# Optimization experiments

Hardware: AMD Instinct MI355X
Metric: run time of the kernel (lower is better)

Reference implementation:

```python
import jax, jax.numpy as jnp
import numpy as np

B, S, D = 32, 512, 768
EPS = 1e-8  # torch CosineSimilarity eps

def setup_inputs() -> dict:
    key = jax.random.key(0)
    k1, k2, k3, k4 = jax.random.split(key, 4)
    emb1 = jax.random.normal(k1, (B, S, D), jnp.float32)
    emb2 = jax.random.normal(k2, (B, S, D), jnp.float32)
    mask1 = jax.random.randint(k3, (B, S), 0, 2).astype(jnp.int32)
    mask2 = jax.random.randint(k4, (B, S), 0, 2).astype(jnp.int32)
    return {"emb1": emb1, "emb2": emb2, "mask1": mask1, "mask2": mask2}

def reference(emb1, emb2, mask1, mask2):
    # normalize token embeddings (cosine sim = dot of unit vectors)
    n1 = emb1 / jnp.maximum(jnp.linalg.norm(emb1, axis=-1, keepdims=True), EPS)
    n2 = emb2 / jnp.maximum(jnp.linalg.norm(emb2, axis=-1, keepdims=True), EPS)
    # full pairwise cosine similarity: [B, S1, S2]
    sim = jnp.einsum('bid,bjd->bij', n1, n2)
    m1 = mask1.astype(sim.dtype)
    m2 = mask2.astype(sim.dtype)
    valid = m1[:, :, None] * m2[:, None, :]
    neg_inf = jnp.asarray(-jnp.inf, sim.dtype)
    masked = jnp.where(valid > 0, sim, neg_inf)
    # row max over valid cols; rows with no valid token contribute 0
    row_max = jnp.where(m1 > 0, jnp.max(masked, axis=2), 0.0)  # [B, S1]
    col_max = jnp.where(m2 > 0, jnp.max(masked, axis=1), 0.0)  # [B, S2]
    denom = jnp.sum(m1, axis=1) + jnp.sum(m2, axis=1)          # n1 + n2
    score = (jnp.sum(row_max, axis=1) + jnp.sum(col_max, axis=1)) / jnp.maximum(denom, 1.0)
    return score  # [B]
```

## Files before the change

kernel.cpp:

```cpp
#include <hip/hip_runtime.h>

#define BB 32
#define SS 512
#define DD 768
#define NROW (BB * SS)

typedef float f32x4 __attribute__((ext_vector_type(4)));
typedef short bf16x8 __attribute__((ext_vector_type(8)));

__device__ __forceinline__ unsigned fkey(float f) {
  unsigned u = __float_as_uint(f);
  return (u & 0x80000000u) ? ~u : (u | 0x80000000u);
}
__device__ __forceinline__ float fdecode(unsigned k) {
  return __uint_as_float((k & 0x80000000u) ? (k & 0x7fffffffu) : ~k);
}
__device__ __forceinline__ unsigned short cvt_bf16(float f) {
  unsigned u = __float_as_uint(f);
  u += 0x7fffu + ((u >> 16) & 1u);
  return (unsigned short)(u >> 16);
}

__global__ __launch_bounds__(256) void norm_cvt_kernel(
    const float* __restrict__ emb1, const float* __restrict__ emb2,
    unsigned short* __restrict__ wsA, unsigned short* __restrict__ wsB,
    unsigned* __restrict__ rowkey, unsigned* __restrict__ colkey) {
  int wave = blockIdx.x * 4 + (threadIdx.x >> 6);
  int lane = threadIdx.x & 63;
  int half = wave >> 14;
  int r = wave & (NROW - 1);
  const float* src = (half ? emb2 : emb1) + (size_t)r * DD;
  float4 v[3];
  float s = 0.f;
#pragma unroll
  for (int q = 0; q < 3; ++q) {
    v[q] = ((const float4*)src)[q * 64 + lane];
    s += v[q].x * v[q].x + v[q].y * v[q].y + v[q].z * v[q].z + v[q].w * v[q].w;
  }
#pragma unroll
  for (int m = 1; m < 64; m <<= 1) s += __shfl_xor(s, m);
  float inv = 1.0f / fmaxf(sqrtf(s), 1e-8f);
  unsigned short* dst = (half ? wsB : wsA) + (size_t)r * DD;
  int base = ((lane >> 4) << 6) + (((((lane >> 1) & 7) ^ (r & 7))) << 3) + ((lane & 1) << 2);
#pragma unroll
  for (int q = 0; q < 3; ++q) {
    ushort4 u;
    u.x = cvt_bf16(v[q].x * inv); u.y = cvt_bf16(v[q].y * inv);
    u.z = cvt_bf16(v[q].z * inv); u.w = cvt_bf16(v[q].w * inv);
    *(ushort4*)(dst + q * 256 + base) = u;
  }
  if (lane == 0) {
    if (half == 0) rowkey[r] = 0x007fffffu;
    else           colkey[r] = 0x007fffffu;
  }
}

__global__ __launch_bounds__(256) void simmax_kernel(
    const unsigned short* __restrict__ wsA, const unsigned short* __restrict__ wsB,
    const int* __restrict__ mask1, const int* __restrict__ mask2,
    unsigned* __restrict__ rowkey, unsigned* __restrict__ colkey) {
  int x = blockIdx.x;
  int b = (x & 7) + (((x >> 3) & 3) << 3);
  int tile = x >> 5;
  int i0 = (tile >> 2) << 7;
  int j0 = (tile & 3) << 7;
  __shared__ __align__(16) unsigned short sA[2][128 * 64];
  __shared__ __align__(16) unsigned short sB[2][128 * 64];
  __shared__ int sM1[128], sM2[128];
  int t = threadIdx.x, l = t & 63, wid = t >> 6, wr = wid >> 1, wc = wid & 1;
  if (t < 128) sM1[t] = mask1[b * SS + i0 + t];
  else sM2[t - 128] = mask2[b * SS + j0 + (t - 128)];
  const unsigned short* gA = wsA + (size_t)(b * SS + i0) * DD;
  const unsigned short* gB = wsB + (size_t)(b * SS + j0) * DD;
  int rsub = l >> 3, csub = l & 7;

  f32x4 acc[4][4] = {};

#define STAGE(buf, k0)                                                              \
  {                                                                                 \
    _Pragma("unroll") for (int j = 0; j < 4; ++j) {                                 \
      int rowblk = (wid * 4 + j) * 8;                                               \
      const unsigned short* ga = gA + (size_t)(rowblk + rsub) * DD + (k0) + csub * 8; \
      const unsigned short* gb = gB + (size_t)(rowblk + rsub) * DD + (k0) + csub * 8; \
      __builtin_amdgcn_global_load_lds(                                             \
          (const __attribute__((address_space(1))) unsigned int*)ga,                \
          (__attribute__((address_space(3))) unsigned int*)&sA[buf][rowblk * 64],   \
          16, 0, 0);                                                                \
      __builtin_amdgcn_global_load_lds(                                             \
          (const __attribute__((address_space(1))) unsigned int*)gb,                \
          (__attribute__((address_space(3))) unsigned int*)&sB[buf][rowblk * 64],   \
          16, 0, 0);                                                                \
    }                                                                               \
  }

  STAGE(0, 0);
  __syncthreads();
  int cur = 0;
#pragma unroll 1
  for (int tk = 0; tk < 12; ++tk) {
    if (tk < 11) STAGE(cur ^ 1, (tk + 1) * 64);
#pragma unroll
    for (int kk = 0; kk < 2; ++kk) {
      bf16x8 af[4], bfr[4];
#pragma unroll
      for (int mi = 0; mi < 4; ++mi) {
        int r = wr * 64 + mi * 16 + (l & 15);
        int ch = (kk << 2) + (l >> 4);
        af[mi] = *(const bf16x8*)(&sA[cur][(r << 6) + ((ch ^ (r & 7)) << 3)]);
      }
#pragma unroll
      for (int ni = 0; ni < 4; ++ni) {
        int r = wc * 64 + ni * 16 + (l & 15);
        int ch = (kk << 2) + (l >> 4);
        bfr[ni] = *(const bf16x8*)(&sB[cur][(r << 6) + ((ch ^ (r & 7)) << 3)]);
      }
#pragma unroll
      for (int mi = 0; mi < 4; ++mi)
#pragma unroll
        for (int ni = 0; ni < 4; ++ni)
          acc[mi][ni] = __builtin_amdgcn_mfma_f32_16x16x32_bf16(af[mi], bfr[ni], acc[mi][ni], 0, 0, 0);
    }
    __syncthreads();
    cur ^= 1;
  }

  const float NEG = -__builtin_inff();
  float rmax[4][4], cmax[4];
#pragma unroll
  for (int mi = 0; mi < 4; ++mi)
#pragma unroll
    for (int rg = 0; rg < 4; ++rg) rmax[mi][rg] = NEG;
#pragma unroll
  for (int ni = 0; ni < 4; ++ni) cmax[ni] = NEG;

#pragma unroll
  for (int mi = 0; mi < 4; ++mi) {
#pragma unroll
    for (int ni = 0; ni < 4; ++ni) {
#pragma unroll
      for (int rg = 0; rg < 4; ++rg) {
        int rl = wr * 64 + mi * 16 + (l >> 4) * 4 + rg;
        int cl = wc * 64 + ni * 16 + (l & 15);
        float v = acc[mi][ni][rg];
        v = (sM1[rl] && sM2[cl]) ? v : NEG;
        rmax[mi][rg] = fmaxf(rmax[mi][rg], v);
        cmax[ni] = fmaxf(cmax[ni], v);
      }
    }
  }
#pragma unroll
  for (int mi = 0; mi < 4; ++mi)
#pragma unroll
    for (int rg = 0; rg < 4; ++rg) {
      float v = rmax[mi][rg];
      v = fmaxf(v, __shfl_xor(v, 1));
      v = fmaxf(v, __shfl_xor(v, 2));
      v = fmaxf(v, __shfl_xor(v, 4));
      v = fmaxf(v, __shfl_xor(v, 8));
      rmax[mi][rg] = v;
    }
#pragma unroll
  for (int ni = 0; ni < 4; ++ni) {
    float v = cmax[ni];
    v = fmaxf(v, __shfl_xor(v, 16));
    v = fmaxf(v, __shfl_xor(v, 32));
    cmax[ni] = v;
  }
  int selm = (l >> 2) & 3, selr = l & 3, seln = (l >> 4) & 3;
  float rv = rmax[0][0], cv = cmax[0];
#pragma unroll
  for (int mi = 0; mi < 4; ++mi)
#pragma unroll
    for (int rg = 0; rg < 4; ++rg)
      if (selm == mi && selr == rg) rv = rmax[mi][rg];
#pragma unroll
  for (int ni = 0; ni < 4; ++ni)
    if (seln == ni) cv = cmax[ni];
  int rl = selm * 16 + ((l >> 4) & 3) * 4 + selr;
  int cl = seln * 16 + (l & 15);
  atomicMax(&rowkey[b * SS + i0 + wr * 64 + rl], fkey(rv));
  atomicMax(&colkey[b * SS + j0 + wc * 64 + cl], fkey(cv));
}

__global__ __launch_bounds__(256) void finalize_kernel(
    const int* __restrict__ mask1, const int* __restrict__ mask2,
    const unsigned* __restrict__ rowkey, const unsigned* __restrict__ colkey,
    float* __restrict__ out) {
  int b = blockIdx.x, t = threadIdx.x;
  float sum = 0.f;
  int cnt = 0;
  for (int s = t; s < SS; s += 256) {
    if (mask1[b * SS + s]) { sum += fdecode(rowkey[b * SS + s]); cnt++; }
    if (mask2[b * SS + s]) { sum += fdecode(colkey[b * SS + s]); cnt++; }
  }
#pragma unroll
  for (int m = 1; m < 64; m <<= 1) {
    sum += __shfl_xor(sum, m);
    cnt += __shfl_xor(cnt, m);
  }
  __shared__ float sS[4];
  __shared__ int sC[4];
  int w = t >> 6, lane = t & 63;
  if (lane == 0) { sS[w] = sum; sC[w] = cnt; }
  __syncthreads();
  if (t == 0) {
    float T = sS[0] + sS[1] + sS[2] + sS[3];
    int C = sC[0] + sC[1] + sC[2] + sC[3];
    out[b] = T / fmaxf((float)C, 1.0f);
  }
}

extern "C" void kernel_launch(void* const* d_in, const int* in_sizes, int n_in,
                              void* d_out, int out_size, void* d_ws, size_t ws_size,
                              hipStream_t stream) {
  const float* emb1 = (const float*)d_in[0];
  const float* emb2 = (const float*)d_in[1];
  const int* mask1 = (const int*)d_in[2];
  const int* mask2 = (const int*)d_in[3];
  float* out = (float*)d_out;

  unsigned short* wsA = (unsigned short*)d_ws;
  unsigned short* wsB = wsA + (size_t)NROW * DD;
  unsigned* rowkey = (unsigned*)(wsB + (size_t)NROW * DD);
  unsigned* colkey = rowkey + NROW;

  norm_cvt_kernel<<<8192, 256, 0, stream>>>(emb1, emb2, wsA, wsB, rowkey, colkey);
  simmax_kernel<<<512, 256, 0, stream>>>(wsA, wsB, mask1, mask2, rowkey, colkey);
  finalize_kernel<<<BB, 256, 0, stream>>>(mask1, mask2, rowkey, colkey, out);
}
```

Baseline: 151.2 us.

## Compact valid tokens via mask index lists and skip masked rows and tiles

Adds an index kernel that compacts the valid token positions of each mask into index lists, pads them to whole 128-row tiles, and resets the max keys. The norm kernel now skips masked rows, and the similarity kernel gathers only valid rows through the index lists, so it can exit early on tiles past the valid count and no longer masks inside the epilogue. With about half the tokens valid, this is meant to cut GEMM work and bf16 writes roughly in proportion to the valid fraction. The cost is one extra small kernel launch, gathered (non-contiguous) row loads, and an added index lookup before the atomics; the swizzle moves from the store side to the load side.

New measurement: 152.8 us. No clear change (+1.0%).

```diff
diff --git a/kernel.cpp b/kernel.cpp
--- a/kernel.cpp
+++ b/kernel.cpp
@@ -21,14 +21,42 @@
   return (unsigned short)(u >> 16);
 }
 
+__global__ __launch_bounds__(64) void index_kernel(
+    const int* __restrict__ mask1, const int* __restrict__ mask2,
+    int* __restrict__ idx1, int* __restrict__ idx2,
+    int* __restrict__ nt1, int* __restrict__ nt2,
+    unsigned* __restrict__ rowkey, unsigned* __restrict__ colkey) {
+  int side = blockIdx.x & 1, b = blockIdx.x >> 1;
+  const int* m = (side ? mask2 : mask1) + b * SS;
+  unsigned* key = (side ? colkey : rowkey) + b * SS;
+  int* idx = (side ? idx2 : idx1) + b * SS;
+  int l = threadIdx.x;
+  int nv = 0, lastelem = 0;
+#pragma unroll
+  for (int c = 0; c < 8; ++c) {
+    int e = c * 64 + l;
+    int v = m[e];
+    key[e] = 0x007fffffu;
+    unsigned long long bal = __ballot(v != 0);
+    int pos = nv + __popcll(bal & ((1ull << l) - 1ull));
+    if (v) idx[pos] = e;
+    nv += __popcll(bal);
+    if (bal) lastelem = c * 64 + (63 - __clzll(bal));
+  }
+  int nt = (nv + 127) >> 7;
+  for (int p = nv + l; p < nt * 128; p += 64) idx[p] = lastelem;
+  if (l == 0) (side ? nt2 : nt1)[b] = nt;
+}
+
 __global__ __launch_bounds__(256) void norm_cvt_kernel(
     const float* __restrict__ emb1, const float* __restrict__ emb2,
-    unsigned short* __restrict__ wsA, unsigned short* __restrict__ wsB,
-    unsigned* __restrict__ rowkey, unsigned* __restrict__ colkey) {
+    const int* __restrict__ mask1, const int* __restrict__ mask2,
+    unsigned short* __restrict__ wsA, unsigned short* __restrict__ wsB) {
   int wave = blockIdx.x * 4 + (threadIdx.x >> 6);
   int lane = threadIdx.x & 63;
   int half = wave >> 14;
   int r = wave & (NROW - 1);
+  if ((half ? mask2 : mask1)[r] == 0) return;
   const float* src = (half ? emb2 : emb1) + (size_t)r * DD;
   float4 v[3];
   float s = 0.f;
@@ -41,38 +69,40 @@
   for (int m = 1; m < 64; m <<= 1) s += __shfl_xor(s, m);
   float inv = 1.0f / fmaxf(sqrtf(s), 1e-8f);
   unsigned short* dst = (half ? wsB : wsA) + (size_t)r * DD;
-  int base = ((lane >> 4) << 6) + (((((lane >> 1) & 7) ^ (r & 7))) << 3) + ((lane & 1) << 2);
 #pragma unroll
   for (int q = 0; q < 3; ++q) {
     ushort4 u;
     u.x = cvt_bf16(v[q].x * inv); u.y = cvt_bf16(v[q].y * inv);
     u.z = cvt_bf16(v[q].z * inv); u.w = cvt_bf16(v[q].w * inv);
-    *(ushort4*)(dst + q * 256 + base) = u;
-  }
-  if (lane == 0) {
-    if (half == 0) rowkey[r] = 0x007fffffu;
-    else           colkey[r] = 0x007fffffu;
+    *(ushort4*)(dst + q * 256 + lane * 4) = u;
   }
 }
 
 __global__ __launch_bounds__(256) void simmax_kernel(
     const unsigned short* __restrict__ wsA, const unsigned short* __restrict__ wsB,
-    const int* __restrict__ mask1, const int* __restrict__ mask2,
+    const int* __restrict__ idx1, const int* __restrict__ idx2,
+    const int* __restrict__ nt1, const int* __restrict__ nt2,
     unsigned* __restrict__ rowkey, unsigned* __restrict__ colkey) {
   int x = blockIdx.x;
-  int b = (x & 7) + (((x >> 3) & 3) << 3);
+  int b = x & 31;
   int tile = x >> 5;
-  int i0 = (tile >> 2) << 7;
-  int j0 = (tile & 3) << 7;
+  int ti = tile >> 2, tj = tile & 3;
+  if (ti >= nt1[b] || tj >= nt2[b]) return;
+  int i0 = ti << 7, j0 = tj << 7;
   __shared__ __align__(16) unsigned short sA[2][128 * 64];
   __shared__ __align__(16) unsigned short sB[2][128 * 64];
-  __shared__ int sM1[128], sM2[128];
   int t = threadIdx.x, l = t & 63, wid = t >> 6, wr = wid >> 1, wc = wid & 1;
-  if (t < 128) sM1[t] = mask1[b * SS + i0 + t];
-  else sM2[t - 128] = mask2[b * SS + j0 + (t - 128)];
-  const unsigned short* gA = wsA + (size_t)(b * SS + i0) * DD;
-  const unsigned short* gB = wsB + (size_t)(b * SS + j0) * DD;
   int rsub = l >> 3, csub = l & 7;
+  int ra[4], rb[4];
+#pragma unroll
+  for (int j = 0; j < 4; ++j) {
+    int rowblk = (wid * 4 + j) * 8;
+    ra[j] = idx1[b * SS + i0 + rowblk + rsub];
+    rb[j] = idx2[b * SS + j0 + rowblk + rsub];
+  }
+  const unsigned short* gA = wsA + (size_t)b * SS * DD;
+  const unsigned short* gB = wsB + (size_t)b * SS * DD;
+  int csw = (csub ^ rsub) << 3;
 
   f32x4 acc[4][4] = {};
 
@@ -80,8 +110,8 @@
   {                                                                                 \
     _Pragma("unroll") for (int j = 0; j < 4; ++j) {                                 \
       int rowblk = (wid * 4 + j) * 8;                                               \
-      const unsigned short* ga = gA + (size_t)(rowblk + rsub) * DD + (k0) + csub * 8; \
-      const unsigned short* gb = gB + (size_t)(rowblk + rsub) * DD + (k0) + csub * 8; \
+      const unsigned short* ga = gA + (size_t)ra[j] * DD + (k0) + csw;              \
+      const unsigned short* gb = gB + (size_t)rb[j] * DD + (k0) + csw;              \
       __builtin_amdgcn_global_load_lds(                                             \
           (const __attribute__((address_space(1))) unsigned int*)ga,                \
           (__attribute__((address_space(3))) unsigned int*)&sA[buf][rowblk * 64],   \
@@ -134,20 +164,15 @@
   for (int ni = 0; ni < 4; ++ni) cmax[ni] = NEG;
 
 #pragma unroll
-  for (int mi = 0; mi < 4; ++mi) {
-#pragma unroll
-    for (int ni = 0; ni < 4; ++ni) {
+  for (int mi = 0; mi < 4; ++mi)
+#pragma unroll
+    for (int ni = 0; ni < 4; ++ni)
 #pragma unroll
       for (int rg = 0; rg < 4; ++rg) {
-        int rl = wr * 64 + mi * 16 + (l >> 4) * 4 + rg;
-        int cl = wc * 64 + ni * 16 + (l & 15);
         float v = acc[mi][ni][rg];
-        v = (sM1[rl] && sM2[cl]) ? v : NEG;
         rmax[mi][rg] = fmaxf(rmax[mi][rg], v);
         cmax[ni] = fmaxf(cmax[ni], v);
       }
-    }
-  }
 #pragma unroll
   for (int mi = 0; mi < 4; ++mi)
 #pragma unroll
@@ -178,8 +203,10 @@
     if (seln == ni) cv = cmax[ni];
   int rl = selm * 16 + ((l >> 4) & 3) * 4 + selr;
   int cl = seln * 16 + (l & 15);
-  atomicMax(&rowkey[b * SS + i0 + wr * 64 + rl], fkey(rv));
-  atomicMax(&colkey[b * SS + j0 + wc * 64 + cl], fkey(cv));
+  int orow = idx1[b * SS + i0 + wr * 64 + rl];
+  int ocol = idx2[b * SS + j0 + wc * 64 + cl];
+  atomicMax(&rowkey[b * SS + orow], fkey(rv));
+  atomicMax(&colkey[b * SS + ocol], fkey(cv));
 }
 
 __global__ __launch_bounds__(256) void finalize_kernel(
@@ -223,8 +250,13 @@
   unsigned short* wsB = wsA + (size_t)NROW * DD;
   unsigned* rowkey = (unsigned*)(wsB + (size_t)NROW * DD);
   unsigned* colkey = rowkey + NROW;
-
-  norm_cvt_kernel<<<8192, 256, 0, stream>>>(emb1, emb2, wsA, wsB, rowkey, colkey);
-  simmax_kernel<<<512, 256, 0, stream>>>(wsA, wsB, mask1, mask2, rowkey, colkey);
+  int* idx1 = (int*)(colkey + NROW);
+  int* idx2 = idx1 + NROW;
+  int* nt1 = idx2 + NROW;
+  int* nt2 = nt1 + BB;
+
+  index_kernel<<<64, 64, 0, stream>>>(mask1, mask2, idx1, idx2, nt1, nt2, rowkey, colkey);
+  norm_cvt_kernel<<<8192, 256, 0, stream>>>(emb1, emb2, mask1, mask2, wsA, wsB);
+  simmax_kernel<<<512, 256, 0, stream>>>(wsA, wsB, idx1, idx2, nt1, nt2, rowkey, colkey);
   finalize_kernel<<<BB, 256, 0, stream>>>(mask1, mask2, rowkey, colkey, out);
 }
```
